# Optimization experiments

Hardware: AMD Instinct MI355X
Metric: run time of the kernel (lower is better)

The kernel has to match this reference:

```python
import jax, jax.numpy as jnp
import numpy as np

ITERS = 3

def squash(x, axis=-1):
    norm = jnp.linalg.norm(x, axis=axis, keepdims=True)
    scale = norm ** 2 / (1 + norm ** 2) / (norm + 1e-08)
    return scale * x

def setup_inputs() -> dict:
    key = jax.random.key(0)
    kx, kw = jax.random.split(key)
    x = jax.random.normal(kx, (64, 8000, 8), dtype=jnp.float32)
    W = 0.01 * jax.random.normal(kw, (10, 8000, 16, 8), dtype=jnp.float32)
    return {"x": x, "W": W}

def reference(x, W):
    # u_hat[b,o,i,d] = W[o,i,d,e] @ x[b,i,e]
    u_hat = jnp.einsum('oide,bie->boid', W, x)  # [B, O, I, D]
    temp_u_hat = jax.lax.stop_gradient(u_hat)
    B, O, I, D = u_hat.shape
    b = jnp.zeros((B, O, I, 1), dtype=u_hat.dtype)
    v = jnp.ones((B, O, D), dtype=u_hat.dtype)
    for i in range(ITERS):
        c = jax.nn.softmax(b, axis=1)  # over out_caps
        if i < ITERS - 1:
            s = (c * temp_u_hat).sum(axis=2)       # [B, O, D]
            v = squash(s)
            # agreement: u_hat . v over dim D
            b = b + jnp.einsum('boid,bod->boi', temp_u_hat, v)[..., None]
        else:
            s = (c * u_hat).sum(axis=2)
            v = squash(s)
    return v
```

## Files before the change

kernel.cpp:

```cpp
#include <hip/hip_runtime.h>
#include <hip/hip_fp16.h>
#include <math.h>

#define IN 8000
#define OC 10
#define NUNIT 1000
#define VACC_F (64 * OC * 16)
#define PART_H (64 * OC * 16)

#define REC_B   28672
#define REC_H   14336
#define XOFF_B  20480
#define XOFF_H  10240
#define REC_TOTAL_B ((size_t)NUNIT * REC_B)

typedef __fp16 h2 __attribute__((ext_vector_type(2)));
typedef _Float16 half8 __attribute__((ext_vector_type(8)));
typedef float f32x16 __attribute__((ext_vector_type(16)));

__device__ __forceinline__ h2 asb(unsigned int v) { return __builtin_bit_cast(h2, v); }

__device__ __forceinline__ float dot2(h2 a, h2 b, float c) {
#if __has_builtin(__builtin_amdgcn_fdot2)
    return __builtin_amdgcn_fdot2(a, b, c, false);
#else
    return fmaf((float)a[0], (float)b[0], fmaf((float)a[1], (float)b[1], c));
#endif
}

__device__ __forceinline__ unsigned int pk_rn(float a, float b) {
    return __builtin_bit_cast(unsigned int, __float22half2_rn(make_float2(a, b)));
}

#define GLDS16(gp, lp) __builtin_amdgcn_global_load_lds(                      \
    (const __attribute__((address_space(1))) void*)(gp),                      \
    (__attribute__((address_space(3))) void*)(lp), 16, 0, 0)

__global__ __launch_bounds__(256) void caps_prep(
    const float* __restrict__ W, const float* __restrict__ x,
    __fp16* __restrict__ rec)
{
    const int t   = threadIdx.x;
    const int blk = blockIdx.x;
    if (blk < 1250) {
        const int gt = blk * 256 + t;
#pragma unroll
        for (int k = 0; k < 4; ++k) {
            int g  = gt + k * 320000;
            int u  = g / 1280;
            int r  = g - u * 1280;
            int il = r / 160;
            int rr = r - il * 160;
            int o  = rr >> 4;
            int d  = rr & 15;
            const float* ip = W + ((size_t)o * IN + (size_t)(u * 8 + il)) * 128 + d * 8;
            float4 f0 = *(const float4*)(ip);
            float4 f1 = *(const float4*)(ip + 4);
            uint4 pk = make_uint4(pk_rn(f0.x, f0.y), pk_rn(f0.z, f0.w),
                                  pk_rn(f1.x, f1.y), pk_rn(f1.z, f1.w));
            *(uint4*)(rec + (size_t)u * REC_H + il * 1280 + o * 128 + d * 8) = pk;
        }
    } else {
        const int u    = (blk - 1250) * 4 + (t >> 6);
        const int lane = t & 63;
#pragma unroll
        for (int il = 0; il < 8; ++il) {
            const float* ip = x + ((size_t)lane * IN + (size_t)(u * 8 + il)) * 8;
            float4 f0 = *(const float4*)(ip);
            float4 f1 = *(const float4*)(ip + 4);
            uint4 pk = make_uint4(pk_rn(f0.x, f0.y), pk_rn(f0.z, f0.w),
                                  pk_rn(f1.x, f1.y), pk_rn(f1.z, f1.w));
            *(uint4*)(rec + (size_t)u * REC_H + XOFF_H + il * 512 + lane * 8) = pk;
        }
    }
}

template<int UNIFORM>
__global__ __launch_bounds__(256, 2) void caps_pass(
    const __fp16* __restrict__ rec, const float* __restrict__ Vacc,
    __fp16* __restrict__ part)
{
    __shared__ __align__(16) unsigned char sm[2 * REC_B];
    __shared__ __align__(16) unsigned char zs[16];

    const int t    = threadIdx.x;
    const int w    = t >> 6;
    const int lane = t & 63;
    const int lo   = lane & 31;
    const int hi   = lane >> 5;
    const int bt   = w & 1;
    const int ph   = w >> 1;
    const int b    = bt * 32 + lo;

    if (t < 4) ((unsigned int*)zs)[t] = 0u;

    h2 vh[10][4];
    if (!UNIFORM) {
        const float* vp = Vacc + (size_t)b * (OC * 16);
        const float L2E = 1.44269504f;
#pragma unroll
        for (int o = 0; o < OC; ++o) {
            float4 fa = *(const float4*)(vp + o * 16 + 4 * hi);
            float4 fb = *(const float4*)(vp + o * 16 + 8 + 4 * hi);
            vh[o][0] = asb(pk_rn(fa.x * L2E, fa.y * L2E));
            vh[o][1] = asb(pk_rn(fa.z * L2E, fa.w * L2E));
            vh[o][2] = asb(pk_rn(fb.x * L2E, fb.y * L2E));
            vh[o][3] = asb(pk_rn(fb.z * L2E, fb.w * L2E));
        }
    }

    f32x16 acc[5];
    h2 acch[5][8];
    if (UNIFORM) {
#pragma unroll
        for (int op = 0; op < 5; ++op)
#pragma unroll
            for (int k = 0; k < 16; ++k) acc[op][k] = 0.f;
    } else {
#pragma unroll
        for (int op = 0; op < 5; ++op)
#pragma unroll
            for (int q = 0; q < 8; ++q) acch[op][q] = h2{(__fp16)0.f, (__fp16)0.f};
    }

    f32x16 zc;
#pragma unroll
    for (int k = 0; k < 16; ++k) zc[k] = 0.f;

    const int bid  = blockIdx.x;
    const int grid = gridDim.x;

    auto issue = [&](int st, int bufi) {
        const char* g = (const char*)rec + (size_t)st * REC_B + (size_t)lane * 16;
        unsigned char* lb = sm + bufi * REC_B;
#pragma unroll
        for (int c = 0; c < 7; ++c) {
            const int q = c * 4 + w;
            GLDS16(g + q * 1024, lb + q * 1024);
        }
    };

    issue(bid, 0);
    if (bid + grid < NUNIT) issue(bid + grid, 1);
    __syncthreads();

    int cur = 0;
    for (int st = bid; st < NUNIT; st += grid) {
        const unsigned char* buf = sm + cur * REC_B;

        if (UNIFORM) {
#pragma unroll
            for (int ip = 0; ip < 2; ++ip) {
                const int il0 = ph * 4 + ip * 2;
                half8 xb = *(const half8*)(buf + XOFF_B + (il0 + hi) * 1024 + b * 16);
#pragma unroll
                for (int op = 0; op < 5; ++op) {
                    half8 av = *(const half8*)(buf + (il0 + hi) * 2560 + op * 512 + lo * 16);
                    acc[op] = __builtin_amdgcn_mfma_f32_32x32x16_f16(av, xb, acc[op], 0, 0, 0);
                }
            }
        } else {
#pragma unroll 1
            for (int u = 0; u < 4; ++u) {
                const int il = ph * 4 + u;
                const unsigned char* xaddr = (lane < 32)
                    ? (buf + XOFF_B + il * 1024 + b * 16)
                    : (const unsigned char*)zs;
                half8 xb = *(const half8*)xaddr;

                h2 uh2[5][8];
                float lgf[10];
#pragma unroll
                for (int op = 0; op < 5; ++op) {
                    half8 av = *(const half8*)(buf + il * 2560 + op * 512 + lo * 16);
                    f32x16 C = __builtin_amdgcn_mfma_f32_32x32x16_f16(av, xb, zc, 0, 0, 0);
#pragma unroll
                    for (int q = 0; q < 8; ++q)
                        uh2[op][q] = __builtin_amdgcn_cvt_pkrtz(C[2 * q], C[2 * q + 1]);
                    float l0 = 0.f, l1 = 0.f;
#pragma unroll
                    for (int qq = 0; qq < 4; ++qq) {
                        l0 = dot2(uh2[op][qq],     vh[op * 2][qq],     l0);
                        l1 = dot2(uh2[op][4 + qq], vh[op * 2 + 1][qq], l1);
                    }
                    lgf[op * 2]     = l0;
                    lgf[op * 2 + 1] = l1;
                }
#pragma unroll
                for (int pp = 0; pp < 5; ++pp) {
                    h2 lp = asb(pk_rn(lgf[2 * pp], lgf[2 * pp + 1]));
                    int ob = __shfl_xor(__builtin_bit_cast(int, lp), 32);
                    h2 s2 = lp + __builtin_bit_cast(h2, ob);
                    lgf[2 * pp]     = (float)s2[0];
                    lgf[2 * pp + 1] = (float)s2[1];
                }
                float m0 = fmaxf(fmaxf(lgf[0], lgf[1]), lgf[2]);
                float m1 = fmaxf(fmaxf(lgf[3], lgf[4]), lgf[5]);
                float m2 = fmaxf(fmaxf(lgf[6], lgf[7]), lgf[8]);
                float mx = fmaxf(fmaxf(m0, m1), fmaxf(m2, lgf[9]));
                float pe[10];
#pragma unroll
                for (int o = 0; o < OC; ++o)
                    pe[o] = __builtin_amdgcn_exp2f(lgf[o] - mx);
                float s01 = pe[0] + pe[1], s23 = pe[2] + pe[3];
                float s45 = pe[4] + pe[5], s67 = pe[6] + pe[7];
                float s89 = pe[8] + pe[9];
                float se = ((s01 + s23) + (s45 + s67)) + s89;
                float rs = __builtin_amdgcn_rcpf(se);
#pragma unroll
                for (int op = 0; op < 5; ++op) {
                    float c0 = pe[op * 2] * rs;
                    float c1 = pe[op * 2 + 1] * rs;
                    h2 ch0 = __builtin_amdgcn_cvt_pkrtz(c0, c0);
                    h2 ch1 = __builtin_amdgcn_cvt_pkrtz(c1, c1);
#pragma unroll
                    for (int q = 0; q < 4; ++q) {
                        acch[op][q]     = ch0 * uh2[op][q]     + acch[op][q];
                        acch[op][4 + q] = ch1 * uh2[op][4 + q] + acch[op][4 + q];
                    }
                }
            }
        }

        const int nxt = st + 2 * grid;
        if (nxt < NUNIT) {
            __syncthreads();
            issue(nxt, cur);
            __syncthreads();
        }
        cur ^= 1;
    }

    float* red = (float*)sm;
#pragma unroll 1
    for (int phase = 0; phase < 2; ++phase) {
        __syncthreads();
        if (ph == phase) {
#pragma unroll
            for (int op = 0; op < 5; ++op)
#pragma unroll
                for (int q = 0; q < 8; ++q) {
                    const int o  = op * 2 + (q >> 2);
                    const int d0 = 2 * (q & 1) + 8 * ((q >> 1) & 1) + 4 * hi;
                    float e0, e1;
                    if (UNIFORM) { e0 = acc[op][2 * q]; e1 = acc[op][2 * q + 1]; }
                    else         { e0 = (float)acch[op][q][0]; e1 = (float)acch[op][q][1]; }
                    float* p = &red[(size_t)b * 164 + o * 16 + d0];
                    if (phase == 0) {
                        *(float2*)p = make_float2(e0, e1);
                    } else {
                        float2 v2 = *(const float2*)p;
                        v2.x += e0; v2.y += e1;
                        *(float2*)p = v2;
                    }
                }
        }
    }
    __syncthreads();
    unsigned int* dst = (unsigned int*)part;
    for (int q = t; q < PART_H / 2; q += 256) {
        int bo = q >> 3;
        int u8 = q & 7;
        int bb = bo / 10;
        int oo = bo - bb * 10;
        float2 v2 = *(const float2*)&red[(size_t)bb * 164 + oo * 16 + u8 * 2];
        dst[(size_t)(bo * grid + bid) * 8 + u8] = pk_rn(v2.x, v2.y);
    }
}

__global__ __launch_bounds__(256) void caps_reduce(
    const __fp16* __restrict__ part, float* __restrict__ Vacc,
    float* __restrict__ out, int nchunk, int mode, float scale)
{
    const int bo = blockIdx.x;
    const int t  = threadIdx.x;
    const int d2 = t & 3;
    const int s  = t >> 2;

    const unsigned int* p32 = (const unsigned int*)part + (size_t)bo * nchunk * 8;
    float4 a = make_float4(0.f, 0.f, 0.f, 0.f);
    for (int c = s; c < nchunk; c += 64) {
        uint2 v = *(const uint2*)(p32 + (size_t)c * 8 + d2 * 2);
        h2 lov = asb(v.x), hiv = asb(v.y);
        a.x += (float)lov[0]; a.y += (float)lov[1];
        a.z += (float)hiv[0]; a.w += (float)hiv[1];
    }
#pragma unroll
    for (int m = 4; m <= 32; m <<= 1) {
        a.x += __shfl_xor(a.x, m); a.y += __shfl_xor(a.y, m);
        a.z += __shfl_xor(a.z, m); a.w += __shfl_xor(a.w, m);
    }
    __shared__ float red[4][16];
    const int wv = t >> 6;
    if ((t & 63) < 4) {
        red[wv][d2 * 4 + 0] = a.x; red[wv][d2 * 4 + 1] = a.y;
        red[wv][d2 * 4 + 2] = a.z; red[wv][d2 * 4 + 3] = a.w;
    }
    __syncthreads();
    if (t < 16) {
        float sv = (red[0][t] + red[1][t] + red[2][t] + red[3][t]) * scale;
        float n2 = sv * sv;
#pragma unroll
        for (int m = 1; m < 16; m <<= 1) n2 += __shfl_xor(n2, m);
        float norm = sqrtf(n2);
        float scl  = n2 / (1.f + n2) / (norm + 1e-8f);
        float v = scl * sv;
        if (mode == 2)      out[bo * 16 + t] = v;
        else if (mode == 0) Vacc[bo * 16 + t] = v;
        else                Vacc[bo * 16 + t] += v;
    }
}

extern "C" void kernel_launch(void* const* d_in, const int* in_sizes, int n_in,
                              void* d_out, int out_size, void* d_ws, size_t ws_size,
                              hipStream_t stream) {
    const float* x = (const float*)d_in[0];
    const float* W = (const float*)d_in[1];
    float* out = (float*)d_out;

    char* ws = (char*)d_ws;
    float*  Vacc = (float*)ws;
    __fp16* rec  = (__fp16*)(ws + VACC_F * sizeof(float));
    __fp16* part = (__fp16*)(ws + VACC_F * sizeof(float) + REC_TOTAL_B);

    size_t head = VACC_F * sizeof(float) + REC_TOTAL_B;
    size_t avail = (ws_size > head) ? ws_size - head : 0;
    long slots = (long)(avail / (PART_H * sizeof(__fp16)));
    int grid = (int)((slots < 500) ? slots : 500);
    if (grid < 1) grid = 1;

    caps_prep<<<1500, 256, 0, stream>>>(W, x, rec);

    caps_pass<1><<<grid, 256, 0, stream>>>(rec, Vacc, part);
    caps_reduce<<<640, 256, 0, stream>>>(part, Vacc, out, grid, 0, 0.1f);
    caps_pass<0><<<grid, 256, 0, stream>>>(rec, Vacc, part);
    caps_reduce<<<640, 256, 0, stream>>>(part, Vacc, out, grid, 1, 1.0f);
    caps_pass<0><<<grid, 256, 0, stream>>>(rec, Vacc, part);
    caps_reduce<<<640, 256, 0, stream>>>(part, Vacc, out, grid, 2, 1.0f);
}
```

Measured before the change: 161.6 us.

## Fuse prep, routing passes and reductions into one cooperative persistent kernel

Replaces seven kernel launches (prep, three passes, three reductions) with a single cooperative kernel that uses grid-wide syncs between stages, removing launch gaps and inter-kernel drains. The grid is sized from occupancy queries, capped at 512 and cached in a static. The reductions now run inside the persistent blocks. In exchange, grid.sync barriers cost time and the grid is bounded by co-residency. The prep stage also becomes a grid-strided loop.

Result: slower. 380.2 us (+135.3%).

```diff
diff --git a/kernel.cpp b/kernel.cpp
--- a/kernel.cpp
+++ b/kernel.cpp
@@ -1,6 +1,9 @@
 #include <hip/hip_runtime.h>
+#include <hip/hip_cooperative_groups.h>
 #include <hip/hip_fp16.h>
 #include <math.h>
+
+namespace cg = cooperative_groups;
 
 #define IN 8000
 #define OC 10
@@ -36,52 +39,16 @@
     (const __attribute__((address_space(1))) void*)(gp),                      \
     (__attribute__((address_space(3))) void*)(lp), 16, 0, 0)
 
-__global__ __launch_bounds__(256) void caps_prep(
+__global__ __launch_bounds__(256, 2) void caps_fused(
     const float* __restrict__ W, const float* __restrict__ x,
-    __fp16* __restrict__ rec)
+    __fp16* __restrict__ rec, float* Vacc, __fp16* part,
+    float* __restrict__ out)
 {
-    const int t   = threadIdx.x;
-    const int blk = blockIdx.x;
-    if (blk < 1250) {
-        const int gt = blk * 256 + t;
-#pragma unroll
-        for (int k = 0; k < 4; ++k) {
-            int g  = gt + k * 320000;
-            int u  = g / 1280;
-            int r  = g - u * 1280;
-            int il = r / 160;
-            int rr = r - il * 160;
-            int o  = rr >> 4;
-            int d  = rr & 15;
-            const float* ip = W + ((size_t)o * IN + (size_t)(u * 8 + il)) * 128 + d * 8;
-            float4 f0 = *(const float4*)(ip);
-            float4 f1 = *(const float4*)(ip + 4);
-            uint4 pk = make_uint4(pk_rn(f0.x, f0.y), pk_rn(f0.z, f0.w),
-                                  pk_rn(f1.x, f1.y), pk_rn(f1.z, f1.w));
-            *(uint4*)(rec + (size_t)u * REC_H + il * 1280 + o * 128 + d * 8) = pk;
-        }
-    } else {
-        const int u    = (blk - 1250) * 4 + (t >> 6);
-        const int lane = t & 63;
-#pragma unroll
-        for (int il = 0; il < 8; ++il) {
-            const float* ip = x + ((size_t)lane * IN + (size_t)(u * 8 + il)) * 8;
-            float4 f0 = *(const float4*)(ip);
-            float4 f1 = *(const float4*)(ip + 4);
-            uint4 pk = make_uint4(pk_rn(f0.x, f0.y), pk_rn(f0.z, f0.w),
-                                  pk_rn(f1.x, f1.y), pk_rn(f1.z, f1.w));
-            *(uint4*)(rec + (size_t)u * REC_H + XOFF_H + il * 512 + lane * 8) = pk;
-        }
-    }
-}
-
-template<int UNIFORM>
-__global__ __launch_bounds__(256, 2) void caps_pass(
-    const __fp16* __restrict__ rec, const float* __restrict__ Vacc,
-    __fp16* __restrict__ part)
-{
+    cg::grid_group gg = cg::this_grid();
+
     __shared__ __align__(16) unsigned char sm[2 * REC_B];
     __shared__ __align__(16) unsigned char zs[16];
+    __shared__ float redsm[4][16];
 
     const int t    = threadIdx.x;
     const int w    = t >> 6;
@@ -91,223 +58,253 @@
     const int bt   = w & 1;
     const int ph   = w >> 1;
     const int b    = bt * 32 + lo;
+    const int bid  = blockIdx.x;
+    const int G    = gridDim.x;
+    const int d2   = t & 3;
+    const int s4   = t >> 2;
 
     if (t < 4) ((unsigned int*)zs)[t] = 0u;
 
-    h2 vh[10][4];
-    if (!UNIFORM) {
-        const float* vp = Vacc + (size_t)b * (OC * 16);
-        const float L2E = 1.44269504f;
-#pragma unroll
-        for (int o = 0; o < OC; ++o) {
-            float4 fa = *(const float4*)(vp + o * 16 + 4 * hi);
-            float4 fb = *(const float4*)(vp + o * 16 + 8 + 4 * hi);
-            vh[o][0] = asb(pk_rn(fa.x * L2E, fa.y * L2E));
-            vh[o][1] = asb(pk_rn(fa.z * L2E, fa.w * L2E));
-            vh[o][2] = asb(pk_rn(fb.x * L2E, fb.y * L2E));
-            vh[o][3] = asb(pk_rn(fb.z * L2E, fb.w * L2E));
-        }
+    for (int g = bid * 256 + t; g < 1280000; g += G * 256) {
+        int u  = g / 1280;
+        int r  = g - u * 1280;
+        int il = r / 160;
+        int rr = r - il * 160;
+        int o  = rr >> 4;
+        int d  = rr & 15;
+        const float* ip = W + ((size_t)o * IN + (size_t)(u * 8 + il)) * 128 + d * 8;
+        float4 f0 = *(const float4*)(ip);
+        float4 f1 = *(const float4*)(ip + 4);
+        *(uint4*)(rec + (size_t)u * REC_H + il * 1280 + o * 128 + d * 8) =
+            make_uint4(pk_rn(f0.x, f0.y), pk_rn(f0.z, f0.w),
+                       pk_rn(f1.x, f1.y), pk_rn(f1.z, f1.w));
     }
-
-    f32x16 acc[5];
-    h2 acch[5][8];
-    if (UNIFORM) {
-#pragma unroll
-        for (int op = 0; op < 5; ++op)
-#pragma unroll
-            for (int k = 0; k < 16; ++k) acc[op][k] = 0.f;
-    } else {
-#pragma unroll
-        for (int op = 0; op < 5; ++op)
-#pragma unroll
-            for (int q = 0; q < 8; ++q) acch[op][q] = h2{(__fp16)0.f, (__fp16)0.f};
+    for (int g = bid * 256 + t; g < 512000; g += G * 256) {
+        int i  = g >> 6;
+        int bb = g & 63;
+        const float* ip = x + ((size_t)bb * IN + i) * 8;
+        float4 f0 = *(const float4*)(ip);
+        float4 f1 = *(const float4*)(ip + 4);
+        *(uint4*)(rec + (size_t)(i >> 3) * REC_H + XOFF_H + (i & 7) * 512 + bb * 8) =
+            make_uint4(pk_rn(f0.x, f0.y), pk_rn(f0.z, f0.w),
+                       pk_rn(f1.x, f1.y), pk_rn(f1.z, f1.w));
     }
-
-    f32x16 zc;
-#pragma unroll
-    for (int k = 0; k < 16; ++k) zc[k] = 0.f;
-
-    const int bid  = blockIdx.x;
-    const int grid = gridDim.x;
+    gg.sync();
 
     auto issue = [&](int st, int bufi) {
-        const char* g = (const char*)rec + (size_t)st * REC_B + (size_t)lane * 16;
+        const char* gp = (const char*)rec + (size_t)st * REC_B + (size_t)lane * 16;
         unsigned char* lb = sm + bufi * REC_B;
 #pragma unroll
         for (int c = 0; c < 7; ++c) {
             const int q = c * 4 + w;
-            GLDS16(g + q * 1024, lb + q * 1024);
+            GLDS16(gp + q * 1024, lb + q * 1024);
         }
     };
 
-    issue(bid, 0);
-    if (bid + grid < NUNIT) issue(bid + grid, 1);
-    __syncthreads();
-
-    int cur = 0;
-    for (int st = bid; st < NUNIT; st += grid) {
-        const unsigned char* buf = sm + cur * REC_B;
-
-        if (UNIFORM) {
-#pragma unroll
-            for (int ip = 0; ip < 2; ++ip) {
-                const int il0 = ph * 4 + ip * 2;
-                half8 xb = *(const half8*)(buf + XOFF_B + (il0 + hi) * 1024 + b * 16);
-#pragma unroll
-                for (int op = 0; op < 5; ++op) {
-                    half8 av = *(const half8*)(buf + (il0 + hi) * 2560 + op * 512 + lo * 16);
-                    acc[op] = __builtin_amdgcn_mfma_f32_32x32x16_f16(av, xb, acc[op], 0, 0, 0);
+    for (int it = 0; it < 3; ++it) {
+        issue(bid, 0);
+        if (bid + G < NUNIT) issue(bid + G, 1);
+        __syncthreads();
+
+        float* red = (float*)sm;
+
+        if (it == 0) {
+            f32x16 acc[5];
+#pragma unroll
+            for (int op = 0; op < 5; ++op)
+#pragma unroll
+                for (int k = 0; k < 16; ++k) acc[op][k] = 0.f;
+
+            int cur = 0;
+            for (int st = bid; st < NUNIT; st += G) {
+                const unsigned char* buf = sm + cur * REC_B;
+#pragma unroll
+                for (int ip = 0; ip < 2; ++ip) {
+                    const int il0 = ph * 4 + ip * 2;
+                    half8 xb = *(const half8*)(buf + XOFF_B + (il0 + hi) * 1024 + b * 16);
+#pragma unroll
+                    for (int op = 0; op < 5; ++op) {
+                        half8 av = *(const half8*)(buf + (il0 + hi) * 2560 + op * 512 + lo * 16);
+                        acc[op] = __builtin_amdgcn_mfma_f32_32x32x16_f16(av, xb, acc[op], 0, 0, 0);
+                    }
+                }
+                const int nxt = st + 2 * G;
+                if (nxt < NUNIT) { __syncthreads(); issue(nxt, cur); __syncthreads(); }
+                cur ^= 1;
+            }
+#pragma unroll 1
+            for (int phase = 0; phase < 2; ++phase) {
+                __syncthreads();
+                if (ph == phase) {
+#pragma unroll
+                    for (int op = 0; op < 5; ++op)
+#pragma unroll
+                        for (int q = 0; q < 8; ++q) {
+                            const int o  = op * 2 + (q >> 2);
+                            const int d0 = 2 * (q & 1) + 8 * ((q >> 1) & 1) + 4 * hi;
+                            float e0 = acc[op][2 * q], e1 = acc[op][2 * q + 1];
+                            float* p = &red[(size_t)b * 164 + o * 16 + d0];
+                            if (phase == 0) *(float2*)p = make_float2(e0, e1);
+                            else { float2 v2 = *(const float2*)p; v2.x += e0; v2.y += e1; *(float2*)p = v2; }
+                        }
                 }
             }
         } else {
+            h2 vh[10][4];
+            {
+                const float* vp = Vacc + (size_t)b * (OC * 16);
+                const float L2E = 1.44269504f;
+#pragma unroll
+                for (int o = 0; o < OC; ++o) {
+                    float4 fa = *(const float4*)(vp + o * 16 + 4 * hi);
+                    float4 fb = *(const float4*)(vp + o * 16 + 8 + 4 * hi);
+                    vh[o][0] = asb(pk_rn(fa.x * L2E, fa.y * L2E));
+                    vh[o][1] = asb(pk_rn(fa.z * L2E, fa.w * L2E));
+                    vh[o][2] = asb(pk_rn(fb.x * L2E, fb.y * L2E));
+                    vh[o][3] = asb(pk_rn(fb.z * L2E, fb.w * L2E));
+                }
+            }
+            h2 acch[5][8];
+#pragma unroll
+            for (int op = 0; op < 5; ++op)
+#pragma unroll
+                for (int q = 0; q < 8; ++q) acch[op][q] = h2{(__fp16)0.f, (__fp16)0.f};
+            f32x16 zc;
+#pragma unroll
+            for (int k = 0; k < 16; ++k) zc[k] = 0.f;
+
+            int cur = 0;
+            for (int st = bid; st < NUNIT; st += G) {
+                const unsigned char* buf = sm + cur * REC_B;
 #pragma unroll 1
-            for (int u = 0; u < 4; ++u) {
-                const int il = ph * 4 + u;
-                const unsigned char* xaddr = (lane < 32)
-                    ? (buf + XOFF_B + il * 1024 + b * 16)
-                    : (const unsigned char*)zs;
-                half8 xb = *(const half8*)xaddr;
-
-                h2 uh2[5][8];
-                float lgf[10];
-#pragma unroll
-                for (int op = 0; op < 5; ++op) {
-                    half8 av = *(const half8*)(buf + il * 2560 + op * 512 + lo * 16);
-                    f32x16 C = __builtin_amdgcn_mfma_f32_32x32x16_f16(av, xb, zc, 0, 0, 0);
-#pragma unroll
-                    for (int q = 0; q < 8; ++q)
-                        uh2[op][q] = __builtin_amdgcn_cvt_pkrtz(C[2 * q], C[2 * q + 1]);
-                    float l0 = 0.f, l1 = 0.f;
-#pragma unroll
-                    for (int qq = 0; qq < 4; ++qq) {
-                        l0 = dot2(uh2[op][qq],     vh[op * 2][qq],     l0);
-                        l1 = dot2(uh2[op][4 + qq], vh[op * 2 + 1][qq], l1);
+                for (int u = 0; u < 4; ++u) {
+                    const int il = ph * 4 + u;
+                    const unsigned char* xaddr = (lane < 32)
+                        ? (buf + XOFF_B + il * 1024 + b * 16)
+                        : (const unsigned char*)zs;
+                    half8 xb = *(const half8*)xaddr;
+
+                    h2 uh2[5][8];
+                    float lgf[10];
+#pragma unroll
+                    for (int op = 0; op < 5; ++op) {
+                        half8 av = *(const half8*)(buf + il * 2560 + op * 512 + lo * 16);
+                        f32x16 C = __builtin_amdgcn_mfma_f32_32x32x16_f16(av, xb, zc, 0, 0, 0);
+#pragma unroll
+                        for (int q = 0; q < 8; ++q)
+                            uh2[op][q] = __builtin_amdgcn_cvt_pkrtz(C[2 * q], C[2 * q + 1]);
+                        float l0 = 0.f, l1 = 0.f;
+#pragma unroll
+                        for (int qq = 0; qq < 4; ++qq) {
+                            l0 = dot2(uh2[op][qq],     vh[op * 2][qq],     l0);
+                            l1 = dot2(uh2[op][4 + qq], vh[op * 2 + 1][qq], l1);
+                        }
+                        lgf[op * 2]     = l0;
+                        lgf[op * 2 + 1] = l1;
                     }
-                    lgf[op * 2]     = l0;
-                    lgf[op * 2 + 1] = l1;
-                }
-#pragma unroll
-                for (int pp = 0; pp < 5; ++pp) {
-                    h2 lp = asb(pk_rn(lgf[2 * pp], lgf[2 * pp + 1]));
-                    int ob = __shfl_xor(__builtin_bit_cast(int, lp), 32);
-                    h2 s2 = lp + __builtin_bit_cast(h2, ob);
-                    lgf[2 * pp]     = (float)s2[0];
-                    lgf[2 * pp + 1] = (float)s2[1];
-                }
-                float m0 = fmaxf(fmaxf(lgf[0], lgf[1]), lgf[2]);
-                float m1 = fmaxf(fmaxf(lgf[3], lgf[4]), lgf[5]);
-                float m2 = fmaxf(fmaxf(lgf[6], lgf[7]), lgf[8]);
-                float mx = fmaxf(fmaxf(m0, m1), fmaxf(m2, lgf[9]));
-                float pe[10];
-#pragma unroll
-                for (int o = 0; o < OC; ++o)
-                    pe[o] = __builtin_amdgcn_exp2f(lgf[o] - mx);
-                float s01 = pe[0] + pe[1], s23 = pe[2] + pe[3];
-                float s45 = pe[4] + pe[5], s67 = pe[6] + pe[7];
-                float s89 = pe[8] + pe[9];
-                float se = ((s01 + s23) + (s45 + s67)) + s89;
-                float rs = __builtin_amdgcn_rcpf(se);
-#pragma unroll
-                for (int op = 0; op < 5; ++op) {
-                    float c0 = pe[op * 2] * rs;
-                    float c1 = pe[op * 2 + 1] * rs;
-                    h2 ch0 = __builtin_amdgcn_cvt_pkrtz(c0, c0);
-                    h2 ch1 = __builtin_amdgcn_cvt_pkrtz(c1, c1);
-#pragma unroll
-                    for (int q = 0; q < 4; ++q) {
-                        acch[op][q]     = ch0 * uh2[op][q]     + acch[op][q];
-                        acch[op][4 + q] = ch1 * uh2[op][4 + q] + acch[op][4 + q];
+#pragma unroll
+                    for (int pp = 0; pp < 5; ++pp) {
+                        h2 lp = asb(pk_rn(lgf[2 * pp], lgf[2 * pp + 1]));
+                        int ob = __shfl_xor(__builtin_bit_cast(int, lp), 32);
+                        h2 s2 = lp + __builtin_bit_cast(h2, ob);
+                        lgf[2 * pp]     = (float)s2[0];
+                        lgf[2 * pp + 1] = (float)s2[1];
                     }
+                    float m0 = fmaxf(fmaxf(lgf[0], lgf[1]), lgf[2]);
+                    float m1 = fmaxf(fmaxf(lgf[3], lgf[4]), lgf[5]);
+                    float m2 = fmaxf(fmaxf(lgf[6], lgf[7]), lgf[8]);
+                    float mx = fmaxf(fmaxf(m0, m1), fmaxf(m2, lgf[9]));
+                    float pe[10];
+#pragma unroll
+                    for (int o = 0; o < OC; ++o)
+                        pe[o] = __builtin_amdgcn_exp2f(lgf[o] - mx);
+                    float s01 = pe[0] + pe[1], s23 = pe[2] + pe[3];
+                    float s45 = pe[4] + pe[5], s67 = pe[6] + pe[7];
+                    float s89 = pe[8] + pe[9];
+                    float se = ((s01 + s23) + (s45 + s67)) + s89;
+                    float rs = __builtin_amdgcn_rcpf(se);
+#pragma unroll
+                    for (int op = 0; op < 5; ++op) {
+                        float c0 = pe[op * 2] * rs;
+                        float c1 = pe[op * 2 + 1] * rs;
+                        h2 ch0 = __builtin_amdgcn_cvt_pkrtz(c0, c0);
+                        h2 ch1 = __builtin_amdgcn_cvt_pkrtz(c1, c1);
+#pragma unroll
+                        for (int q = 0; q < 4; ++q) {
+                            acch[op][q]     = ch0 * uh2[op][q]     + acch[op][q];
+                            acch[op][4 + q] = ch1 * uh2[op][4 + q] + acch[op][4 + q];
+                        }
+                    }
+                }
+                const int nxt = st + 2 * G;
+                if (nxt < NUNIT) { __syncthreads(); issue(nxt, cur); __syncthreads(); }
+                cur ^= 1;
+            }
+#pragma unroll 1
+            for (int phase = 0; phase < 2; ++phase) {
+                __syncthreads();
+                if (ph == phase) {
+#pragma unroll
+                    for (int op = 0; op < 5; ++op)
+#pragma unroll
+                        for (int q = 0; q < 8; ++q) {
+                            const int o  = op * 2 + (q >> 2);
+                            const int d0 = 2 * (q & 1) + 8 * ((q >> 1) & 1) + 4 * hi;
+                            float e0 = (float)acch[op][q][0], e1 = (float)acch[op][q][1];
+                            float* p = &red[(size_t)b * 164 + o * 16 + d0];
+                            if (phase == 0) *(float2*)p = make_float2(e0, e1);
+                            else { float2 v2 = *(const float2*)p; v2.x += e0; v2.y += e1; *(float2*)p = v2; }
+                        }
                 }
             }
         }
-
-        const int nxt = st + 2 * grid;
-        if (nxt < NUNIT) {
+        __syncthreads();
+        unsigned int* dst = (unsigned int*)part;
+        for (int q = t; q < PART_H / 2; q += 256) {
+            int bo = q >> 3;
+            int u8 = q & 7;
+            int bb = bo / 10;
+            int oo = bo - bb * 10;
+            float2 v2 = *(const float2*)&red[(size_t)bb * 164 + oo * 16 + u8 * 2];
+            dst[(size_t)(bo * G + bid) * 8 + u8] = pk_rn(v2.x, v2.y);
+        }
+        gg.sync();
+
+        const float scale = (it == 0) ? 0.1f : 1.0f;
+        for (int bo = bid; bo < 640; bo += G) {
             __syncthreads();
-            issue(nxt, cur);
+            const unsigned int* p32 = (const unsigned int*)part + (size_t)bo * G * 8;
+            float4 a = make_float4(0.f, 0.f, 0.f, 0.f);
+            for (int c = s4; c < G; c += 64) {
+                uint2 v = *(const uint2*)(p32 + (size_t)c * 8 + d2 * 2);
+                h2 lov = asb(v.x), hiv = asb(v.y);
+                a.x += (float)lov[0]; a.y += (float)lov[1];
+                a.z += (float)hiv[0]; a.w += (float)hiv[1];
+            }
+#pragma unroll
+            for (int m = 4; m <= 32; m <<= 1) {
+                a.x += __shfl_xor(a.x, m); a.y += __shfl_xor(a.y, m);
+                a.z += __shfl_xor(a.z, m); a.w += __shfl_xor(a.w, m);
+            }
+            if (lane < 4) {
+                redsm[w][d2 * 4 + 0] = a.x; redsm[w][d2 * 4 + 1] = a.y;
+                redsm[w][d2 * 4 + 2] = a.z; redsm[w][d2 * 4 + 3] = a.w;
+            }
             __syncthreads();
+            if (t < 16) {
+                float sv = (redsm[0][t] + redsm[1][t] + redsm[2][t] + redsm[3][t]) * scale;
+                float n2 = sv * sv;
+#pragma unroll
+                for (int m = 1; m < 16; m <<= 1) n2 += __shfl_xor(n2, m);
+                float norm = sqrtf(n2);
+                float scl  = n2 / (1.f + n2) / (norm + 1e-8f);
+                float v = scl * sv;
+                if (it == 2)      out[bo * 16 + t] = v;
+                else if (it == 0) Vacc[bo * 16 + t] = v;
+                else              Vacc[bo * 16 + t] += v;
+            }
         }
-        cur ^= 1;
-    }
-
-    float* red = (float*)sm;
-#pragma unroll 1
-    for (int phase = 0; phase < 2; ++phase) {
-        __syncthreads();
-        if (ph == phase) {
-#pragma unroll
-            for (int op = 0; op < 5; ++op)
-#pragma unroll
-                for (int q = 0; q < 8; ++q) {
-                    const int o  = op * 2 + (q >> 2);
-                    const int d0 = 2 * (q & 1) + 8 * ((q >> 1) & 1) + 4 * hi;
-                    float e0, e1;
-                    if (UNIFORM) { e0 = acc[op][2 * q]; e1 = acc[op][2 * q + 1]; }
-                    else         { e0 = (float)acch[op][q][0]; e1 = (float)acch[op][q][1]; }
-                    float* p = &red[(size_t)b * 164 + o * 16 + d0];
-                    if (phase == 0) {
-                        *(float2*)p = make_float2(e0, e1);
-                    } else {
-                        float2 v2 = *(const float2*)p;
-                        v2.x += e0; v2.y += e1;
-                        *(float2*)p = v2;
-                    }
-                }
-        }
-    }
-    __syncthreads();
-    unsigned int* dst = (unsigned int*)part;
-    for (int q = t; q < PART_H / 2; q += 256) {
-        int bo = q >> 3;
-        int u8 = q & 7;
-        int bb = bo / 10;
-        int oo = bo - bb * 10;
-        float2 v2 = *(const float2*)&red[(size_t)bb * 164 + oo * 16 + u8 * 2];
-        dst[(size_t)(bo * grid + bid) * 8 + u8] = pk_rn(v2.x, v2.y);
-    }
-}
-
-__global__ __launch_bounds__(256) void caps_reduce(
-    const __fp16* __restrict__ part, float* __restrict__ Vacc,
-    float* __restrict__ out, int nchunk, int mode, float scale)
-{
-    const int bo = blockIdx.x;
-    const int t  = threadIdx.x;
-    const int d2 = t & 3;
-    const int s  = t >> 2;
-
-    const unsigned int* p32 = (const unsigned int*)part + (size_t)bo * nchunk * 8;
-    float4 a = make_float4(0.f, 0.f, 0.f, 0.f);
-    for (int c = s; c < nchunk; c += 64) {
-        uint2 v = *(const uint2*)(p32 + (size_t)c * 8 + d2 * 2);
-        h2 lov = asb(v.x), hiv = asb(v.y);
-        a.x += (float)lov[0]; a.y += (float)lov[1];
-        a.z += (float)hiv[0]; a.w += (float)hiv[1];
-    }
-#pragma unroll
-    for (int m = 4; m <= 32; m <<= 1) {
-        a.x += __shfl_xor(a.x, m); a.y += __shfl_xor(a.y, m);
-        a.z += __shfl_xor(a.z, m); a.w += __shfl_xor(a.w, m);
-    }
-    __shared__ float red[4][16];
-    const int wv = t >> 6;
-    if ((t & 63) < 4) {
-        red[wv][d2 * 4 + 0] = a.x; red[wv][d2 * 4 + 1] = a.y;
-        red[wv][d2 * 4 + 2] = a.z; red[wv][d2 * 4 + 3] = a.w;
-    }
-    __syncthreads();
-    if (t < 16) {
-        float sv = (red[0][t] + red[1][t] + red[2][t] + red[3][t]) * scale;
-        float n2 = sv * sv;
-#pragma unroll
-        for (int m = 1; m < 16; m <<= 1) n2 += __shfl_xor(n2, m);
-        float norm = sqrtf(n2);
-        float scl  = n2 / (1.f + n2) / (norm + 1e-8f);
-        float v = scl * sv;
-        if (mode == 2)      out[bo * 16 + t] = v;
-        else if (mode == 0) Vacc[bo * 16 + t] = v;
-        else                Vacc[bo * 16 + t] += v;
+        gg.sync();
     }
 }
 
@@ -323,18 +320,26 @@
     __fp16* rec  = (__fp16*)(ws + VACC_F * sizeof(float));
     __fp16* part = (__fp16*)(ws + VACC_F * sizeof(float) + REC_TOTAL_B);
 
+    static int grid_cached = 0;
+    if (grid_cached == 0) {
+        int maxb = 0;
+        if (hipOccupancyMaxActiveBlocksPerMultiprocessor(&maxb, caps_fused, 256, 0)
+                != hipSuccess || maxb < 1)
+            maxb = 1;
+        long g = (long)maxb * 256;
+        if (g > 512) g = 512;
+        grid_cached = (int)g;
+    }
+    long grid = grid_cached;
+
     size_t head = VACC_F * sizeof(float) + REC_TOTAL_B;
     size_t avail = (ws_size > head) ? ws_size - head : 0;
     long slots = (long)(avail / (PART_H * sizeof(__fp16)));
-    int grid = (int)((slots < 500) ? slots : 500);
+    if (grid > slots) grid = slots;
     if (grid < 1) grid = 1;
 
-    caps_prep<<<1500, 256, 0, stream>>>(W, x, rec);
-
-    caps_pass<1><<<grid, 256, 0, stream>>>(rec, Vacc, part);
-    caps_reduce<<<640, 256, 0, stream>>>(part, Vacc, out, grid, 0, 0.1f);
-    caps_pass<0><<<grid, 256, 0, stream>>>(rec, Vacc, part);
-    caps_reduce<<<640, 256, 0, stream>>>(part, Vacc, out, grid, 1, 1.0f);
-    caps_pass<0><<<grid, 256, 0, stream>>>(rec, Vacc, part);
-    caps_reduce<<<640, 256, 0, stream>>>(part, Vacc, out, grid, 2, 1.0f);
+    void* args[] = {(void*)&W, (void*)&x, (void*)&rec, (void*)&Vacc,
+                    (void*)&part, (void*)&out};
+    hipLaunchCooperativeKernel((const void*)caps_fused, dim3((unsigned)grid),
+                               dim3(256), args, 0, stream);
 }
```

## Fuse fp16 repacking of W and x into the first routing pass kernel

Applied to the files above, without the earlier changes.

The separate prep kernel that converts W and x to fp16 records is removed. The first (uniform) routing pass now loads fp32 W and x per unit directly, converts them into shared memory, writes the packed record to global memory for later passes, and computes its MFMA accumulation from shared memory. This saves one launch and one full read of the packed record. In exchange, the fused pass loses its double-buffered async global-to-LDS prefetch, and each unit now does synchronous loads and conversion between barriers.

After: 168.2 us. +4.1%, slower.

```diff
diff --git a/kernel.cpp b/kernel.cpp
--- a/kernel.cpp
+++ b/kernel.cpp
@@ -36,52 +36,11 @@
     (const __attribute__((address_space(1))) void*)(gp),                      \
     (__attribute__((address_space(3))) void*)(lp), 16, 0, 0)
 
-__global__ __launch_bounds__(256) void caps_prep(
+__global__ __launch_bounds__(256, 2) void caps_pass0(
     const float* __restrict__ W, const float* __restrict__ x,
-    __fp16* __restrict__ rec)
+    __fp16* __restrict__ rec, __fp16* __restrict__ part)
 {
-    const int t   = threadIdx.x;
-    const int blk = blockIdx.x;
-    if (blk < 1250) {
-        const int gt = blk * 256 + t;
-#pragma unroll
-        for (int k = 0; k < 4; ++k) {
-            int g  = gt + k * 320000;
-            int u  = g / 1280;
-            int r  = g - u * 1280;
-            int il = r / 160;
-            int rr = r - il * 160;
-            int o  = rr >> 4;
-            int d  = rr & 15;
-            const float* ip = W + ((size_t)o * IN + (size_t)(u * 8 + il)) * 128 + d * 8;
-            float4 f0 = *(const float4*)(ip);
-            float4 f1 = *(const float4*)(ip + 4);
-            uint4 pk = make_uint4(pk_rn(f0.x, f0.y), pk_rn(f0.z, f0.w),
-                                  pk_rn(f1.x, f1.y), pk_rn(f1.z, f1.w));
-            *(uint4*)(rec + (size_t)u * REC_H + il * 1280 + o * 128 + d * 8) = pk;
-        }
-    } else {
-        const int u    = (blk - 1250) * 4 + (t >> 6);
-        const int lane = t & 63;
-#pragma unroll
-        for (int il = 0; il < 8; ++il) {
-            const float* ip = x + ((size_t)lane * IN + (size_t)(u * 8 + il)) * 8;
-            float4 f0 = *(const float4*)(ip);
-            float4 f1 = *(const float4*)(ip + 4);
-            uint4 pk = make_uint4(pk_rn(f0.x, f0.y), pk_rn(f0.z, f0.w),
-                                  pk_rn(f1.x, f1.y), pk_rn(f1.z, f1.w));
-            *(uint4*)(rec + (size_t)u * REC_H + XOFF_H + il * 512 + lane * 8) = pk;
-        }
-    }
-}
-
-template<int UNIFORM>
-__global__ __launch_bounds__(256, 2) void caps_pass(
-    const __fp16* __restrict__ rec, const float* __restrict__ Vacc,
-    __fp16* __restrict__ part)
-{
-    __shared__ __align__(16) unsigned char sm[2 * REC_B];
-    __shared__ __align__(16) unsigned char zs[16];
+    __shared__ __align__(16) unsigned char sm[41984];
 
     const int t    = threadIdx.x;
     const int w    = t >> 6;
@@ -91,144 +50,61 @@
     const int bt   = w & 1;
     const int ph   = w >> 1;
     const int b    = bt * 32 + lo;
-
-    if (t < 4) ((unsigned int*)zs)[t] = 0u;
-
-    h2 vh[10][4];
-    if (!UNIFORM) {
-        const float* vp = Vacc + (size_t)b * (OC * 16);
-        const float L2E = 1.44269504f;
-#pragma unroll
-        for (int o = 0; o < OC; ++o) {
-            float4 fa = *(const float4*)(vp + o * 16 + 4 * hi);
-            float4 fb = *(const float4*)(vp + o * 16 + 8 + 4 * hi);
-            vh[o][0] = asb(pk_rn(fa.x * L2E, fa.y * L2E));
-            vh[o][1] = asb(pk_rn(fa.z * L2E, fa.w * L2E));
-            vh[o][2] = asb(pk_rn(fb.x * L2E, fb.y * L2E));
-            vh[o][3] = asb(pk_rn(fb.z * L2E, fb.w * L2E));
-        }
-    }
-
-    f32x16 acc[5];
-    h2 acch[5][8];
-    if (UNIFORM) {
-#pragma unroll
-        for (int op = 0; op < 5; ++op)
-#pragma unroll
-            for (int k = 0; k < 16; ++k) acc[op][k] = 0.f;
-    } else {
-#pragma unroll
-        for (int op = 0; op < 5; ++op)
-#pragma unroll
-            for (int q = 0; q < 8; ++q) acch[op][q] = h2{(__fp16)0.f, (__fp16)0.f};
-    }
-
-    f32x16 zc;
-#pragma unroll
-    for (int k = 0; k < 16; ++k) zc[k] = 0.f;
-
     const int bid  = blockIdx.x;
     const int grid = gridDim.x;
 
-    auto issue = [&](int st, int bufi) {
-        const char* g = (const char*)rec + (size_t)st * REC_B + (size_t)lane * 16;
-        unsigned char* lb = sm + bufi * REC_B;
-#pragma unroll
-        for (int c = 0; c < 7; ++c) {
-            const int q = c * 4 + w;
-            GLDS16(g + q * 1024, lb + q * 1024);
-        }
-    };
-
-    issue(bid, 0);
-    if (bid + grid < NUNIT) issue(bid + grid, 1);
-    __syncthreads();
-
-    int cur = 0;
+    unsigned short* Wl = (unsigned short*)sm;
+    unsigned short* xl = (unsigned short*)(sm + XOFF_B);
+
+    f32x16 acc[5];
+#pragma unroll
+    for (int op = 0; op < 5; ++op)
+#pragma unroll
+        for (int k = 0; k < 16; ++k) acc[op][k] = 0.f;
+
     for (int st = bid; st < NUNIT; st += grid) {
-        const unsigned char* buf = sm + cur * REC_B;
-
-        if (UNIFORM) {
-#pragma unroll
-            for (int ip = 0; ip < 2; ++ip) {
-                const int il0 = ph * 4 + ip * 2;
-                half8 xb = *(const half8*)(buf + XOFF_B + (il0 + hi) * 1024 + b * 16);
-#pragma unroll
-                for (int op = 0; op < 5; ++op) {
-                    half8 av = *(const half8*)(buf + (il0 + hi) * 2560 + op * 512 + lo * 16);
-                    acc[op] = __builtin_amdgcn_mfma_f32_32x32x16_f16(av, xb, acc[op], 0, 0, 0);
-                }
+        const int is = st * 8;
+        __syncthreads();
+        for (int j = t; j < 8 * 320; j += 256) {
+            int il = j >> 5;
+            il = j / 320;
+            int r  = j - il * 320;
+            int o  = r >> 5;
+            int f  = r & 31;
+            float4 w4 = *(const float4*)(W + (size_t)o * (IN * 128) +
+                                         (size_t)(is + il) * 128 + f * 4);
+            *(uint2*)&Wl[il * 1280 + o * 128 + f * 4] =
+                make_uint2(pk_rn(w4.x, w4.y), pk_rn(w4.z, w4.w));
+        }
+        for (int j = t; j < 8 * 128; j += 256) {
+            int bb = j >> 4;
+            int r  = j & 15;
+            int il = r >> 1;
+            int hh = r & 1;
+            float4 x4 = *(const float4*)(x + (size_t)bb * (IN * 8) +
+                                         (size_t)(is + il) * 8 + hh * 4);
+            *(uint2*)&xl[il * 512 + bb * 8 + hh * 4] =
+                make_uint2(pk_rn(x4.x, x4.y), pk_rn(x4.z, x4.w));
+        }
+        __syncthreads();
+
+        {
+            const uint4* srcv = (const uint4*)sm;
+            uint4* dstv = (uint4*)((char*)rec + (size_t)st * REC_B);
+#pragma unroll
+            for (int c = 0; c < 7; ++c) dstv[c * 256 + t] = srcv[c * 256 + t];
+        }
+
+#pragma unroll
+        for (int ip = 0; ip < 2; ++ip) {
+            const int il0 = ph * 4 + ip * 2;
+            half8 xb = *(const half8*)(sm + XOFF_B + (il0 + hi) * 1024 + b * 16);
+#pragma unroll
+            for (int op = 0; op < 5; ++op) {
+                half8 av = *(const half8*)(sm + (il0 + hi) * 2560 + op * 512 + lo * 16);
+                acc[op] = __builtin_amdgcn_mfma_f32_32x32x16_f16(av, xb, acc[op], 0, 0, 0);
             }
-        } else {
-#pragma unroll 1
-            for (int u = 0; u < 4; ++u) {
-                const int il = ph * 4 + u;
-                const unsigned char* xaddr = (lane < 32)
-                    ? (buf + XOFF_B + il * 1024 + b * 16)
-                    : (const unsigned char*)zs;
-                half8 xb = *(const half8*)xaddr;
-
-                h2 uh2[5][8];
-                float lgf[10];
-#pragma unroll
-                for (int op = 0; op < 5; ++op) {
-                    half8 av = *(const half8*)(buf + il * 2560 + op * 512 + lo * 16);
-                    f32x16 C = __builtin_amdgcn_mfma_f32_32x32x16_f16(av, xb, zc, 0, 0, 0);
-#pragma unroll
-                    for (int q = 0; q < 8; ++q)
-                        uh2[op][q] = __builtin_amdgcn_cvt_pkrtz(C[2 * q], C[2 * q + 1]);
-                    float l0 = 0.f, l1 = 0.f;
-#pragma unroll
-                    for (int qq = 0; qq < 4; ++qq) {
-                        l0 = dot2(uh2[op][qq],     vh[op * 2][qq],     l0);
-                        l1 = dot2(uh2[op][4 + qq], vh[op * 2 + 1][qq], l1);
-                    }
-                    lgf[op * 2]     = l0;
-                    lgf[op * 2 + 1] = l1;
-                }
-#pragma unroll
-                for (int pp = 0; pp < 5; ++pp) {
-                    h2 lp = asb(pk_rn(lgf[2 * pp], lgf[2 * pp + 1]));
-                    int ob = __shfl_xor(__builtin_bit_cast(int, lp), 32);
-                    h2 s2 = lp + __builtin_bit_cast(h2, ob);
-                    lgf[2 * pp]     = (float)s2[0];
-                    lgf[2 * pp + 1] = (float)s2[1];
-                }
-                float m0 = fmaxf(fmaxf(lgf[0], lgf[1]), lgf[2]);
-                float m1 = fmaxf(fmaxf(lgf[3], lgf[4]), lgf[5]);
-                float m2 = fmaxf(fmaxf(lgf[6], lgf[7]), lgf[8]);
-                float mx = fmaxf(fmaxf(m0, m1), fmaxf(m2, lgf[9]));
-                float pe[10];
-#pragma unroll
-                for (int o = 0; o < OC; ++o)
-                    pe[o] = __builtin_amdgcn_exp2f(lgf[o] - mx);
-                float s01 = pe[0] + pe[1], s23 = pe[2] + pe[3];
-                float s45 = pe[4] + pe[5], s67 = pe[6] + pe[7];
-                float s89 = pe[8] + pe[9];
-                float se = ((s01 + s23) + (s45 + s67)) + s89;
-                float rs = __builtin_amdgcn_rcpf(se);
-#pragma unroll
-                for (int op = 0; op < 5; ++op) {
-                    float c0 = pe[op * 2] * rs;
-                    float c1 = pe[op * 2 + 1] * rs;
-                    h2 ch0 = __builtin_amdgcn_cvt_pkrtz(c0, c0);
-                    h2 ch1 = __builtin_amdgcn_cvt_pkrtz(c1, c1);
-#pragma unroll
-                    for (int q = 0; q < 4; ++q) {
-                        acch[op][q]     = ch0 * uh2[op][q]     + acch[op][q];
-                        acch[op][4 + q] = ch1 * uh2[op][4 + q] + acch[op][4 + q];
-                    }
-                }
-            }
-        }
-
-        const int nxt = st + 2 * grid;
-        if (nxt < NUNIT) {
-            __syncthreads();
-            issue(nxt, cur);
-            __syncthreads();
-        }
-        cur ^= 1;
+        }
     }
 
     float* red = (float*)sm;
@@ -242,17 +118,10 @@
                 for (int q = 0; q < 8; ++q) {
                     const int o  = op * 2 + (q >> 2);
                     const int d0 = 2 * (q & 1) + 8 * ((q >> 1) & 1) + 4 * hi;
-                    float e0, e1;
-                    if (UNIFORM) { e0 = acc[op][2 * q]; e1 = acc[op][2 * q + 1]; }
-                    else         { e0 = (float)acch[op][q][0]; e1 = (float)acch[op][q][1]; }
+                    float e0 = acc[op][2 * q], e1 = acc[op][2 * q + 1];
                     float* p = &red[(size_t)b * 164 + o * 16 + d0];
-                    if (phase == 0) {
-                        *(float2*)p = make_float2(e0, e1);
-                    } else {
-                        float2 v2 = *(const float2*)p;
-                        v2.x += e0; v2.y += e1;
-                        *(float2*)p = v2;
-                    }
+                    if (phase == 0) *(float2*)p = make_float2(e0, e1);
+                    else { float2 v2 = *(const float2*)p; v2.x += e0; v2.y += e1; *(float2*)p = v2; }
                 }
         }
     }
@@ -268,6 +137,170 @@
     }
 }
 
+__global__ __launch_bounds__(256, 2) void caps_pass(
+    const __fp16* __restrict__ rec, const float* __restrict__ Vacc,
+    __fp16* __restrict__ part)
+{
+    __shared__ __align__(16) unsigned char sm[2 * REC_B];
+    __shared__ __align__(16) unsigned char zs[16];
+
+    const int t    = threadIdx.x;
+    const int w    = t >> 6;
+    const int lane = t & 63;
+    const int lo   = lane & 31;
+    const int hi   = lane >> 5;
+    const int bt   = w & 1;
+    const int ph   = w >> 1;
+    const int b    = bt * 32 + lo;
+
+    if (t < 4) ((unsigned int*)zs)[t] = 0u;
+
+    h2 vh[10][4];
+    {
+        const float* vp = Vacc + (size_t)b * (OC * 16);
+        const float L2E = 1.44269504f;
+#pragma unroll
+        for (int o = 0; o < OC; ++o) {
+            float4 fa = *(const float4*)(vp + o * 16 + 4 * hi);
+            float4 fb = *(const float4*)(vp + o * 16 + 8 + 4 * hi);
+            vh[o][0] = asb(pk_rn(fa.x * L2E, fa.y * L2E));
+            vh[o][1] = asb(pk_rn(fa.z * L2E, fa.w * L2E));
+            vh[o][2] = asb(pk_rn(fb.x * L2E, fb.y * L2E));
+            vh[o][3] = asb(pk_rn(fb.z * L2E, fb.w * L2E));
+        }
+    }
+
+    h2 acch[5][8];
+#pragma unroll
+    for (int op = 0; op < 5; ++op)
+#pragma unroll
+        for (int q = 0; q < 8; ++q) acch[op][q] = h2{(__fp16)0.f, (__fp16)0.f};
+
+    f32x16 zc;
+#pragma unroll
+    for (int k = 0; k < 16; ++k) zc[k] = 0.f;
+
+    const int bid  = blockIdx.x;
+    const int grid = gridDim.x;
+
+    auto issue = [&](int st, int bufi) {
+        const char* g = (const char*)rec + (size_t)st * REC_B + (size_t)lane * 16;
+        unsigned char* lb = sm + bufi * REC_B;
+#pragma unroll
+        for (int c = 0; c < 7; ++c) {
+            const int q = c * 4 + w;
+            GLDS16(g + q * 1024, lb + q * 1024);
+        }
+    };
+
+    issue(bid, 0);
+    if (bid + grid < NUNIT) issue(bid + grid, 1);
+    __syncthreads();
+
+    int cur = 0;
+    for (int st = bid; st < NUNIT; st += grid) {
+        const unsigned char* buf = sm + cur * REC_B;
+
+#pragma unroll 1
+        for (int u = 0; u < 4; ++u) {
+            const int il = ph * 4 + u;
+            const unsigned char* xaddr = (lane < 32)
+                ? (buf + XOFF_B + il * 1024 + b * 16)
+                : (const unsigned char*)zs;
+            half8 xb = *(const half8*)xaddr;
+
+            h2 uh2[5][8];
+            float lgf[10];
+#pragma unroll
+            for (int op = 0; op < 5; ++op) {
+                half8 av = *(const half8*)(buf + il * 2560 + op * 512 + lo * 16);
+                f32x16 C = __builtin_amdgcn_mfma_f32_32x32x16_f16(av, xb, zc, 0, 0, 0);
+#pragma unroll
+                for (int q = 0; q < 8; ++q)
+                    uh2[op][q] = __builtin_amdgcn_cvt_pkrtz(C[2 * q], C[2 * q + 1]);
+                float l0 = 0.f, l1 = 0.f;
+#pragma unroll
+                for (int qq = 0; qq < 4; ++qq) {
+                    l0 = dot2(uh2[op][qq],     vh[op * 2][qq],     l0);
+                    l1 = dot2(uh2[op][4 + qq], vh[op * 2 + 1][qq], l1);
+                }
+                lgf[op * 2]     = l0;
+                lgf[op * 2 + 1] = l1;
+            }
+#pragma unroll
+            for (int pp = 0; pp < 5; ++pp) {
+                h2 lp = asb(pk_rn(lgf[2 * pp], lgf[2 * pp + 1]));
+                int ob = __shfl_xor(__builtin_bit_cast(int, lp), 32);
+                h2 s2 = lp + __builtin_bit_cast(h2, ob);
+                lgf[2 * pp]     = (float)s2[0];
+                lgf[2 * pp + 1] = (float)s2[1];
+            }
+            float m0 = fmaxf(fmaxf(lgf[0], lgf[1]), lgf[2]);
+            float m1 = fmaxf(fmaxf(lgf[3], lgf[4]), lgf[5]);
+            float m2 = fmaxf(fmaxf(lgf[6], lgf[7]), lgf[8]);
+            float mx = fmaxf(fmaxf(m0, m1), fmaxf(m2, lgf[9]));
+            float pe[10];
+#pragma unroll
+            for (int o = 0; o < OC; ++o)
+                pe[o] = __builtin_amdgcn_exp2f(lgf[o] - mx);
+            float s01 = pe[0] + pe[1], s23 = pe[2] + pe[3];
+            float s45 = pe[4] + pe[5], s67 = pe[6] + pe[7];
+            float s89 = pe[8] + pe[9];
+            float se = ((s01 + s23) + (s45 + s67)) + s89;
+            float rs = __builtin_amdgcn_rcpf(se);
+#pragma unroll
+            for (int op = 0; op < 5; ++op) {
+                float c0 = pe[op * 2] * rs;
+                float c1 = pe[op * 2 + 1] * rs;
+                h2 ch0 = __builtin_amdgcn_cvt_pkrtz(c0, c0);
+                h2 ch1 = __builtin_amdgcn_cvt_pkrtz(c1, c1);
+#pragma unroll
+                for (int q = 0; q < 4; ++q) {
+                    acch[op][q]     = ch0 * uh2[op][q]     + acch[op][q];
+                    acch[op][4 + q] = ch1 * uh2[op][4 + q] + acch[op][4 + q];
+                }
+            }
+        }
+
+        const int nxt = st + 2 * grid;
+        if (nxt < NUNIT) {
+            __syncthreads();
+            issue(nxt, cur);
+            __syncthreads();
+        }
+        cur ^= 1;
+    }
+
+    float* red = (float*)sm;
+#pragma unroll 1
+    for (int phase = 0; phase < 2; ++phase) {
+        __syncthreads();
+        if (ph == phase) {
+#pragma unroll
+            for (int op = 0; op < 5; ++op)
+#pragma unroll
+                for (int q = 0; q < 8; ++q) {
+                    const int o  = op * 2 + (q >> 2);
+                    const int d0 = 2 * (q & 1) + 8 * ((q >> 1) & 1) + 4 * hi;
+                    float e0 = (float)acch[op][q][0], e1 = (float)acch[op][q][1];
+                    float* p = &red[(size_t)b * 164 + o * 16 + d0];
+                    if (phase == 0) *(float2*)p = make_float2(e0, e1);
+                    else { float2 v2 = *(const float2*)p; v2.x += e0; v2.y += e1; *(float2*)p = v2; }
+                }
+        }
+    }
+    __syncthreads();
+    unsigned int* dst = (unsigned int*)part;
+    for (int q = t; q < PART_H / 2; q += 256) {
+        int bo = q >> 3;
+        int u8 = q & 7;
+        int bb = bo / 10;
+        int oo = bo - bb * 10;
+        float2 v2 = *(const float2*)&red[(size_t)bb * 164 + oo * 16 + u8 * 2];
+        dst[(size_t)(bo * grid + bid) * 8 + u8] = pk_rn(v2.x, v2.y);
+    }
+}
+
 __global__ __launch_bounds__(256) void caps_reduce(
     const __fp16* __restrict__ part, float* __restrict__ Vacc,
     float* __restrict__ out, int nchunk, int mode, float scale)
@@ -329,12 +362,10 @@
     int grid = (int)((slots < 500) ? slots : 500);
     if (grid < 1) grid = 1;
 
-    caps_prep<<<1500, 256, 0, stream>>>(W, x, rec);
-
-    caps_pass<1><<<grid, 256, 0, stream>>>(rec, Vacc, part);
+    caps_pass0<<<grid, 256, 0, stream>>>(W, x, rec, part);
     caps_reduce<<<640, 256, 0, stream>>>(part, Vacc, out, grid, 0, 0.1f);
-    caps_pass<0><<<grid, 256, 0, stream>>>(rec, Vacc, part);
+    caps_pass<<<grid, 256, 0, stream>>>(rec, Vacc, part);
     caps_reduce<<<640, 256, 0, stream>>>(part, Vacc, out, grid, 1, 1.0f);
-    caps_pass<0><<<grid, 256, 0, stream>>>(rec, Vacc, part);
+    caps_pass<<<grid, 256, 0, stream>>>(rec, Vacc, part);
     caps_reduce<<<640, 256, 0, stream>>>(part, Vacc, out, grid, 2, 1.0f);
 }
```
